# Optimization experiments

Hardware: AMD Instinct MI355X
Metric: run time of the kernel (lower is better)

Reference implementation:

```python
import jax, jax.numpy as jnp
import numpy as np

B, Nres, TOP_K, NUM_RBF = 2, 2048, 30, 16
MAX_REL = 32  # positional clip range -> 2*32+2 = 66 classes


def _gather_nodes(nodes, idx):
    # nodes: [B, N, ...], idx: [B, N, K] -> [B, N, K, ...]
    return jax.vmap(lambda n, i: n[i])(nodes, idx)


def _rbf(D):
    # D: [..., ] -> [..., NUM_RBF]; mu in [2, 22], sigma = 20/16
    mu = jnp.linspace(2.0, 22.0, NUM_RBF)
    sigma = (22.0 - 2.0) / NUM_RBF
    return jnp.exp(-(((D[..., None] - mu) / sigma) ** 2))


def setup_inputs() -> dict:
    key = jax.random.key(0)
    ks = jax.random.split(key, 4)
    X = jax.random.normal(ks[0], (B, Nres, 4, 3), dtype=jnp.float32) * 3.0
    mask = jnp.ones((B, Nres), dtype=jnp.float32)
    residue_idx = jnp.broadcast_to(jnp.arange(Nres, dtype=jnp.int32)[None], (B, Nres))
    chain_labels = jnp.zeros((B, Nres), dtype=jnp.int32)
    w_pos = jax.random.normal(ks[1], (66, 16), dtype=jnp.float32) * 0.05
    b_pos = jax.random.normal(ks[2], (16,), dtype=jnp.float32) * 0.05
    w_edge = jax.random.normal(ks[3], (416, 128), dtype=jnp.float32) * 0.05
    ln_gamma = jnp.ones((128,), dtype=jnp.float32)
    ln_beta = jnp.zeros((128,), dtype=jnp.float32)
    return dict(X=X, mask=mask, residue_idx=residue_idx, chain_labels=chain_labels,
                w_pos=w_pos, b_pos=b_pos, w_edge=w_edge, ln_gamma=ln_gamma, ln_beta=ln_beta)


def reference(X, mask, residue_idx, chain_labels, w_pos, b_pos, w_edge, ln_gamma, ln_beta):
    # virtual C-beta from N, C, Ca (atom order in X: N=0, C=1, Ca=2, O=3)
    b = X[:, :, 2, :] - X[:, :, 0, :]
    c = X[:, :, 1, :] - X[:, :, 2, :]
    a = jnp.cross(b, c)
    Cb = -0.58273431 * a + 0.56802827 * b - 0.54067466 * c + X[:, :, 2, :]
    N_, C, Ca, O = X[:, :, 0, :], X[:, :, 1, :], X[:, :, 2, :], X[:, :, 3, :]

    # masked kNN on C atoms (ProteinFeatures._dist)
    m2 = mask[:, None, :] * mask[:, :, None]                       # [B,N,N]
    dX = C[:, None, :, :] - C[:, :, None, :]
    D = m2 * jnp.sqrt(jnp.sum(dX ** 2, -1) + 1e-6)
    D_max = jnp.max(D, -1, keepdims=True)
    D_adj = D + (1.0 - m2) * D_max
    neg, E_idx = jax.lax.top_k(-D_adj, TOP_K)                      # smallest-k
    D_neighbors = -neg                                             # [B,N,K]

    # 25-channel RBF features; gather neighbor coords instead of NxN per pair
    atoms = jnp.stack([N_, Ca, Cb, C, O], 0)                       # [5,B,N,3]
    gathered = jax.vmap(lambda A: _gather_nodes(A, E_idx))(atoms)  # [5,B,N,K,3]
    # pair order follows torch source: NN,CaCa,CbCb,CN,CCa,CCb,NCa,NCb,CbCa,
    # NC,CaC,CbC,CaN,CbN,CaCb,OO,CO,OC,NO,ON,CbO,OCa,OCb,CaO  (0=N,1=Ca,2=Cb,3=C,4=O)
    pa = jnp.array([0, 1, 2, 3, 3, 3, 0, 0, 2, 0, 1, 2, 1, 2, 1, 4, 3, 4, 0, 4, 2, 4, 4, 1])
    pb = jnp.array([0, 1, 2, 0, 1, 2, 1, 2, 1, 3, 3, 3, 0, 0, 2, 4, 4, 3, 4, 0, 4, 1, 2, 4])
    A_sel = atoms[pa]                                              # [24,B,N,3]
    Bn_sel = gathered[pb]                                          # [24,B,N,K,3]
    Dp = jnp.sqrt(jnp.sum((A_sel[:, :, :, None, :] - Bn_sel) ** 2, -1) + 1e-6)
    RBF_all = jnp.concatenate([_rbf(D_neighbors)[None], _rbf(Dp)], 0)  # [25,B,N,K,16]
    RBF_all = jnp.moveaxis(RBF_all, 0, 3).reshape(B, Nres, TOP_K, 25 * NUM_RBF)

    # positional encodings over gathered offsets / chain match
    offset = residue_idx[:, :, None] - _gather_nodes(residue_idx, E_idx)   # [B,N,K]
    E_chains = (chain_labels[:, :, None] == _gather_nodes(chain_labels, E_idx)).astype(jnp.int32)
    d = jnp.clip(offset + MAX_REL, 0, 2 * MAX_REL) * E_chains + (1 - E_chains) * (2 * MAX_REL + 1)
    E_pos = w_pos[d] + b_pos                                       # one_hot @ W == gather

    # edge embedding + layernorm
    E = jnp.concatenate([E_pos, RBF_all], -1) @ w_edge             # [B,N,K,128]
    mu = E.mean(-1, keepdims=True)
    var = E.var(-1, keepdims=True)
    E = (E - mu) / jnp.sqrt(var + 1e-5) * ln_gamma + ln_beta
    return E, E_idx
```

## Files before the change

kernel.cpp:

```cpp
#include <hip/hip_runtime.h>
#include <hip/hip_bf16.h>
#include <stdint.h>

#define BB    2
#define NRES  2048
#define TOPK  30
#define NRBF  16
#define NFEAT 416
#define NCH   128
#define NS8   108
#define NKT   13
#define RPB   2

typedef __attribute__((ext_vector_type(4))) float f32x4;
typedef unsigned long long u64;

__constant__ int c_pa[24] = {0,1,2,3,3,3,0,0,2,0,1,2,1,2,1,4,3,4,0,4,2,4,4,1};
__constant__ int c_pb[24] = {0,1,2,0,1,2,1,2,1,3,3,3,0,0,2,4,4,3,4,0,4,1,2,4};

static __device__ __forceinline__ unsigned pack4_fp8(float f0, float f1, float f2, float f3) {
  unsigned r = 0;
  r = __builtin_amdgcn_cvt_pk_fp8_f32(f0, f1, r, false);
  r = __builtin_amdgcn_cvt_pk_fp8_f32(f2, f3, r, true);
  return r;
}
static __device__ __forceinline__ u64 umin64(u64 a, u64 b) { return a < b ? a : b; }
static __device__ __forceinline__ u64 umax64(u64 a, u64 b) { return a > b ? a : b; }

__global__ __launch_bounds__(256) void prep_kernel(const float* __restrict__ X,
                                                   const float* __restrict__ w_edge,
                                                   float* __restrict__ atoms,
                                                   float4* __restrict__ Cpk,
                                                   unsigned* __restrict__ wB8) {
  if (blockIdx.x < 16) {
    int id = blockIdx.x * 256 + threadIdx.x;
    const float* x = X + (size_t)id * 12;
    float nx = x[0], ny = x[1], nz = x[2];
    float cx = x[3], cy = x[4], cz = x[5];
    float ax = x[6], ay = x[7], az = x[8];
    float ox = x[9], oy = x[10], oz = x[11];
    float bx = ax - nx, by = ay - ny, bz = az - nz;
    float ccx = cx - ax, ccy = cy - ay, ccz = cz - az;
    float crx = by * ccz - bz * ccy;
    float cry = bz * ccx - bx * ccz;
    float crz = bx * ccy - by * ccx;
    float cbx = -0.58273431f * crx + 0.56802827f * bx - 0.54067466f * ccx + ax;
    float cby = -0.58273431f * cry + 0.56802827f * by - 0.54067466f * ccy + ay;
    float cbz = -0.58273431f * crz + 0.56802827f * bz - 0.54067466f * ccz + az;
    float* r = atoms + (size_t)id * 16;
    r[0] = nx;  r[1] = ny;  r[2] = nz;
    r[3] = ax;  r[4] = ay;  r[5] = az;
    r[6] = cbx; r[7] = cby; r[8] = cbz;
    r[9] = cx;  r[10] = cy; r[11] = cz;
    r[12] = ox; r[13] = oy; r[14] = oz;
    r[15] = 0.f;
    Cpk[id] = make_float4(cx, cy, cz, 0.f);
  } else {
    int id = (blockIdx.x - 16) * 256 + threadIdx.x;
    if (id >= NFEAT * NCH / 4) return;
    int bb   = id * 4;
    int j0   = bb & 7;
    int lane = (bb >> 3) & 63;
    int nt   = (bb >> 9) & 7;
    int kt   = bb >> 12;
    int col  = nt * 16 + (lane & 15);
    int kb   = kt * 32 + ((lane >> 4) << 3) + j0;
    wB8[id] = pack4_fp8(w_edge[(size_t)(kb + 0) * NCH + col],
                        w_edge[(size_t)(kb + 1) * NCH + col],
                        w_edge[(size_t)(kb + 2) * NCH + col],
                        w_edge[(size_t)(kb + 3) * NCH + col]);
  }
}

__global__ __launch_bounds__(256) void topk_kernel(const float4* __restrict__ Cpk,
                                                   int* __restrict__ eidx,
                                                   float* __restrict__ dn,
                                                   float* __restrict__ outI) {
  int tid = threadIdx.x;
  int lane = tid & 63;
  int bi = blockIdx.x * 4 + (tid >> 6);
  int b = bi >> 11;
  int i = bi & (NRES - 1);
  const float4* Cb = Cpk + (size_t)b * NRES;
  float4 ci = Cb[i];

  u64 key[4][8];
  u64 g1[4], g2[4];
#pragma unroll
  for (int g = 0; g < 4; ++g) {
    g1[g] = ~0ull; g2[g] = ~0ull;
#pragma unroll
    for (int s = 0; s < 8; ++s) {
      int j = lane + 64 * (g * 8 + s);
      float4 cj = Cb[j];
      float dx = cj.x - ci.x, dy = cj.y - ci.y, dz = cj.z - ci.z;
      float sm = __fadd_rn(__fadd_rn(__fadd_rn(__fmul_rn(dx, dx), __fmul_rn(dy, dy)),
                                     __fmul_rn(dz, dz)), 1e-6f);
      float d = sqrtf(sm);
      u64 kk = ((u64)__float_as_uint(d) << 32) | (unsigned)j;
      key[g][s] = kk;
      if (kk < g1[g]) { g2[g] = g1[g]; g1[g] = kk; }
      else if (kk < g2[g]) g2[g] = kk;
    }
  }

  for (int kk2 = 0; kk2 < TOPK / 2; ++kk2) {
    u64 x1 = umin64(g1[0], g1[1]);
    u64 x2 = umin64(umax64(g1[0], g1[1]), umin64(g2[0], g2[1]));
    u64 y1 = umin64(g1[2], g1[3]);
    u64 y2 = umin64(umax64(g1[2], g1[3]), umin64(g2[2], g2[3]));
    u64 m1 = umin64(x1, y1);
    u64 m2 = umin64(umax64(x1, y1), umin64(x2, y2));
#pragma unroll
    for (int off = 32; off; off >>= 1) {
      u64 o1 = __shfl_xor(m1, off, 64);
      u64 o2 = __shfl_xor(m2, off, 64);
      u64 n1 = umin64(m1, o1);
      u64 n2 = umin64(umax64(m1, o1), umin64(m2, o2));
      m1 = n1; m2 = n2;
    }
    if (lane == 0) {
      int i1 = (int)(unsigned)m1, i2 = (int)(unsigned)m2;
      size_t o = (size_t)bi * TOPK + 2 * kk2;
      eidx[o] = i1;           eidx[o + 1] = i2;
      dn[o]   = __uint_as_float((unsigned)(m1 >> 32));
      dn[o+1] = __uint_as_float((unsigned)(m2 >> 32));
      outI[o] = (float)i1;    outI[o + 1] = (float)i2;
    }
#pragma unroll
    for (int g = 0; g < 4; ++g) {
      bool hit = (g1[g] == m1) | (g1[g] == m2) | (g2[g] == m2);
      if (hit) {
        u64 n1 = ~0ull, n2 = ~0ull;
#pragma unroll
        for (int s = 0; s < 8; ++s) {
          u64 kv = key[g][s];
          if (kv == m1 || kv == m2) { kv = ~0ull; key[g][s] = kv; }
          if (kv < n1) { n2 = n1; n1 = kv; }
          else if (kv < n2) n2 = kv;
        }
        g1[g] = n1; g2[g] = n2;
      }
    }
  }
}

__global__ __launch_bounds__(256) void edge_mfma_kernel(
    const float* __restrict__ atoms, const int* __restrict__ eidx_g,
    const float* __restrict__ dn_g, const int* __restrict__ ridx,
    const int* __restrict__ chain, const float* __restrict__ w_pos,
    const float* __restrict__ b_pos, const unsigned* __restrict__ wB8,
    const float* __restrict__ gamma, const float* __restrict__ beta,
    float* __restrict__ outE) {
  __shared__ __align__(16) unsigned feat8[RPB * 32 * NS8];
  __shared__ float nat[RPB * TOPK][16];
  __shared__ float iat[RPB][16];
  __shared__ float dn_s[RPB * TOPK];
  __shared__ int   dsel[RPB * TOPK];
  __shared__ float2 lnp[RPB][32][4];

  int tid = threadIdx.x;
  int bi0 = blockIdx.x * RPB;
  int b = bi0 >> 11;
  int nq = tid >> 6, lane = tid & 63;
  int q = lane >> 4, ccol = lane & 15;

  if (tid < RPB * TOPK) {
    int gi = bi0 + tid / TOPK;
    int k = tid % TOPK;
    dn_s[tid] = dn_g[(size_t)gi * TOPK + k];
    int j = eidx_g[(size_t)gi * TOPK + k];
    int off = ridx[gi] - ridx[b * NRES + j];
    int ec = (chain[gi] == chain[b * NRES + j]) ? 1 : 0;
    int d = off + 32; d = d < 0 ? 0 : (d > 64 ? 64 : d);
    dsel[tid] = ec ? d : 65;
  }
  if (tid >= 64 && tid < 64 + RPB * 16) {
    int t = tid - 64;
    iat[t >> 4][t & 15] = atoms[((size_t)bi0 + (t >> 4)) * 16 + (t & 15)];
  }
  for (int idx = tid; idx < RPB * TOPK * 16; idx += 256) {
    int e = idx >> 4, f = idx & 15;
    int gi = bi0 + e / TOPK;
    nat[e][f] = atoms[((size_t)(b * NRES) + eidx_g[(size_t)gi * TOPK + (e % TOPK)]) * 16 + f];
  }
  for (int idx = tid; idx < RPB * 2 * NS8; idx += 256) {
    int r = idx / (2 * NS8), rem = idx % (2 * NS8);
    feat8[(r * 32 + 30) * NS8 + rem] = 0u;
  }
  __syncthreads();

  if (tid < RPB * TOPK * 4) {
    int e = tid >> 2, p = tid & 3;
    int f0 = p * 4, ds = dsel[e];
    int r = e / TOPK, k = e % TOPK;
    feat8[(r * 32 + k) * NS8 + p] = pack4_fp8(w_pos[ds * 16 + f0 + 0] + b_pos[f0 + 0],
                                              w_pos[ds * 16 + f0 + 1] + b_pos[f0 + 1],
                                              w_pos[ds * 16 + f0 + 2] + b_pos[f0 + 2],
                                              w_pos[ds * 16 + f0 + 3] + b_pos[f0 + 3]);
  }
  for (int idx = tid; idx < RPB * TOPK * 25; idx += 256) {
    int e = idx / 25, g = idx - e * 25;
    int r = e / TOPK, k = e - r * TOPK;
    float d;
    if (g == 0) {
      d = dn_s[e];
    } else {
      int qq = g - 1;
      const float* A  = &iat[r][c_pa[qq] * 3];
      const float* Bv = &nat[e][c_pb[qq] * 3];
      float dx = A[0] - Bv[0], dy = A[1] - Bv[1], dz = A[2] - Bv[2];
      d = sqrtf(dx * dx + dy * dy + dz * dz + 1e-6f);
    }
    float v[16];
#pragma unroll
    for (int j = 0; j < 16; ++j) {
      float mu = 2.0f + (float)j * (20.0f / 15.0f);
      float t = (d - mu) * 0.8f;
      v[j] = __expf(-t * t);
    }
    uint4 w4 = make_uint4(pack4_fp8(v[0], v[1], v[2], v[3]),
                          pack4_fp8(v[4], v[5], v[6], v[7]),
                          pack4_fp8(v[8], v[9], v[10], v[11]),
                          pack4_fp8(v[12], v[13], v[14], v[15]));
    *(uint4*)&feat8[(r * 32 + k) * NS8 + 4 + 4 * g] = w4;
  }
  __syncthreads();

  const unsigned* ar00 = &feat8[(0 * 32 + ccol) * NS8];
  const unsigned* ar01 = &feat8[(0 * 32 + 16 + ccol) * NS8];
  const unsigned* ar10 = &feat8[(1 * 32 + ccol) * NS8];
  const unsigned* ar11 = &feat8[(1 * 32 + 16 + ccol) * NS8];
  const u64* wBll = (const u64*)wB8;

  f32x4 a000 = {}, a001 = {}, a010 = {}, a011 = {};
  f32x4 a100 = {}, a101 = {}, a110 = {}, a111 = {};
#pragma unroll
  for (int kt = 0; kt < NKT; ++kt) {
    union { unsigned u[2]; long long l; } f00, f01, f10, f11;
    int ao = kt * 8 + q * 2;
    f00.u[0] = ar00[ao]; f00.u[1] = ar00[ao + 1];
    f01.u[0] = ar01[ao]; f01.u[1] = ar01[ao + 1];
    f10.u[0] = ar10[ao]; f10.u[1] = ar10[ao + 1];
    f11.u[0] = ar11[ao]; f11.u[1] = ar11[ao + 1];
    long long b0 = (long long)wBll[(size_t)(kt * 8 + nq * 2 + 0) * 64 + lane];
    long long b1 = (long long)wBll[(size_t)(kt * 8 + nq * 2 + 1) * 64 + lane];
    a000 = __builtin_amdgcn_mfma_f32_16x16x32_fp8_fp8(f00.l, b0, a000, 0, 0, 0);
    a001 = __builtin_amdgcn_mfma_f32_16x16x32_fp8_fp8(f00.l, b1, a001, 0, 0, 0);
    a010 = __builtin_amdgcn_mfma_f32_16x16x32_fp8_fp8(f01.l, b0, a010, 0, 0, 0);
    a011 = __builtin_amdgcn_mfma_f32_16x16x32_fp8_fp8(f01.l, b1, a011, 0, 0, 0);
    a100 = __builtin_amdgcn_mfma_f32_16x16x32_fp8_fp8(f10.l, b0, a100, 0, 0, 0);
    a101 = __builtin_amdgcn_mfma_f32_16x16x32_fp8_fp8(f10.l, b1, a101, 0, 0, 0);
    a110 = __builtin_amdgcn_mfma_f32_16x16x32_fp8_fp8(f11.l, b0, a110, 0, 0, 0);
    a111 = __builtin_amdgcn_mfma_f32_16x16x32_fp8_fp8(f11.l, b1, a111, 0, 0, 0);
  }

#pragma unroll
  for (int r = 0; r < RPB; ++r) {
#pragma unroll
    for (int mh = 0; mh < 2; ++mh) {
#pragma unroll
      for (int reg = 0; reg < 4; ++reg) {
        float v0, v1;
        if (r == 0) { v0 = mh ? a010[reg] : a000[reg]; v1 = mh ? a011[reg] : a001[reg]; }
        else        { v0 = mh ? a110[reg] : a100[reg]; v1 = mh ? a111[reg] : a101[reg]; }
        float s = v0 + v1, ss = v0 * v0 + v1 * v1;
        s  += __shfl_xor(s, 1, 64);  ss += __shfl_xor(ss, 1, 64);
        s  += __shfl_xor(s, 2, 64);  ss += __shfl_xor(ss, 2, 64);
        s  += __shfl_xor(s, 4, 64);  ss += __shfl_xor(ss, 4, 64);
        s  += __shfl_xor(s, 8, 64);  ss += __shfl_xor(ss, 8, 64);
        if (ccol == 0) lnp[r][(mh << 4) + q * 4 + reg][nq] = make_float2(s, ss);
      }
    }
  }
  __syncthreads();

  float g0 = gamma[(nq * 2 + 0) * 16 + ccol], be0 = beta[(nq * 2 + 0) * 16 + ccol];
  float g1 = gamma[(nq * 2 + 1) * 16 + ccol], be1 = beta[(nq * 2 + 1) * 16 + ccol];
#pragma unroll
  for (int r = 0; r < RPB; ++r) {
#pragma unroll
    for (int mh = 0; mh < 2; ++mh) {
#pragma unroll
      for (int reg = 0; reg < 4; ++reg) {
        int m = (mh << 4) + q * 4 + reg;
        if (m < TOPK) {
          float2 p0 = lnp[r][m][0], p1 = lnp[r][m][1], p2 = lnp[r][m][2], p3 = lnp[r][m][3];
          float s = (p0.x + p1.x) + (p2.x + p3.x);
          float ss = (p0.y + p1.y) + (p2.y + p3.y);
          float mu = s * (1.0f / 128.0f);
          float var = ss * (1.0f / 128.0f) - mu * mu;
          float rstd = rsqrtf(var + 1e-5f);
          float va, vb;
          if (r == 0) { va = mh ? a010[reg] : a000[reg]; vb = mh ? a011[reg] : a001[reg]; }
          else        { va = mh ? a110[reg] : a100[reg]; vb = mh ? a111[reg] : a101[reg]; }
          float* o = outE + ((size_t)(bi0 + r) * TOPK + m) * NCH + ccol;
          o[(nq * 2 + 0) * 16] = (va - mu) * rstd * g0 + be0;
          o[(nq * 2 + 1) * 16] = (vb - mu) * rstd * g1 + be1;
        }
      }
    }
  }
}

extern "C" void kernel_launch(void* const* d_in, const int* in_sizes, int n_in,
                              void* d_out, int out_size, void* d_ws, size_t ws_size,
                              hipStream_t stream) {
  const float* X      = (const float*)d_in[0];
  const int*   ridx   = (const int*)d_in[2];
  const int*   chain  = (const int*)d_in[3];
  const float* w_pos  = (const float*)d_in[4];
  const float* b_pos  = (const float*)d_in[5];
  const float* w_edge = (const float*)d_in[6];
  const float* gamma  = (const float*)d_in[7];
  const float* beta   = (const float*)d_in[8];

  float* outE = (float*)d_out;
  float* outI = outE + (size_t)BB * NRES * TOPK * NCH;

  char* p = (char*)d_ws;
  float* atoms = (float*)p;                 p += (size_t)BB * NRES * 16 * 4;
  int*   eidx  = (int*)p;                   p += (size_t)BB * NRES * TOPK * 4;
  float* dn    = (float*)p;                 p += (size_t)BB * NRES * TOPK * 4;
  unsigned* wB8 = (unsigned*)p;             p += (size_t)NCH * NFEAT;
  float4* Cpk  = (float4*)p;

  prep_kernel<<<16 + (NFEAT * NCH / 4 + 255) / 256, 256, 0, stream>>>(X, w_edge, atoms, Cpk, wB8);
  topk_kernel<<<BB * NRES / 4, 256, 0, stream>>>(Cpk, eidx, dn, outI);
  edge_mfma_kernel<<<BB * NRES / RPB, 256, 0, stream>>>(atoms, eidx, dn, ridx, chain,
                                                        w_pos, b_pos, wB8, gamma, beta, outE);
}
```

Baseline: 93.81 us.

## Process two query rows per wave in top-k and switch to single-min extraction

Each wavefront in the top-k kernel now handles two query residues, sharing the neighbor coordinate loads, and interleaves their two independent shuffle-reduction chains. Selection goes from extracting two minima per round with a top-2 merge to extracting one minimum per round over 30 rounds, which makes each round simpler. The intent is better instruction-level parallelism and fewer loads per query. The cost is double the key register footprint, raised occupancy pressure (a launch_bounds min-blocks hint of 2 is added), twice as many reduction rounds, and half as many blocks.

```diff
diff --git a/kernel.cpp b/kernel.cpp
--- a/kernel.cpp
+++ b/kernel.cpp
@@ -24,8 +24,6 @@
   r = __builtin_amdgcn_cvt_pk_fp8_f32(f2, f3, r, true);
   return r;
 }
-static __device__ __forceinline__ u64 umin64(u64 a, u64 b) { return a < b ? a : b; }
-static __device__ __forceinline__ u64 umax64(u64 a, u64 b) { return a > b ? a : b; }
 
 __global__ __launch_bounds__(256) void prep_kernel(const float* __restrict__ X,
                                                    const float* __restrict__ w_edge,
@@ -72,74 +70,84 @@
   }
 }
 
-__global__ __launch_bounds__(256) void topk_kernel(const float4* __restrict__ Cpk,
-                                                   int* __restrict__ eidx,
-                                                   float* __restrict__ dn,
-                                                   float* __restrict__ outI) {
+__global__ __launch_bounds__(256, 2) void topk_kernel(const float4* __restrict__ Cpk,
+                                                      int* __restrict__ eidx,
+                                                      float* __restrict__ dn,
+                                                      float* __restrict__ outI) {
   int tid = threadIdx.x;
   int lane = tid & 63;
-  int bi = blockIdx.x * 4 + (tid >> 6);
-  int b = bi >> 11;
-  int i = bi & (NRES - 1);
+  int biA = blockIdx.x * 8 + (tid >> 6) * 2;
+  int biB = biA + 1;
+  int b = biA >> 11;
   const float4* Cb = Cpk + (size_t)b * NRES;
-  float4 ci = Cb[i];
-
-  u64 key[4][8];
-  u64 g1[4], g2[4];
+  float4 ciA = Cb[biA & (NRES - 1)];
+  float4 ciB = Cb[biB & (NRES - 1)];
+
+  u64 keyA[4][8], keyB[4][8];
+  u64 subA[4], subB[4];
 #pragma unroll
   for (int g = 0; g < 4; ++g) {
-    g1[g] = ~0ull; g2[g] = ~0ull;
+    subA[g] = ~0ull; subB[g] = ~0ull;
 #pragma unroll
     for (int s = 0; s < 8; ++s) {
       int j = lane + 64 * (g * 8 + s);
       float4 cj = Cb[j];
-      float dx = cj.x - ci.x, dy = cj.y - ci.y, dz = cj.z - ci.z;
-      float sm = __fadd_rn(__fadd_rn(__fadd_rn(__fmul_rn(dx, dx), __fmul_rn(dy, dy)),
-                                     __fmul_rn(dz, dz)), 1e-6f);
-      float d = sqrtf(sm);
-      u64 kk = ((u64)__float_as_uint(d) << 32) | (unsigned)j;
-      key[g][s] = kk;
-      if (kk < g1[g]) { g2[g] = g1[g]; g1[g] = kk; }
-      else if (kk < g2[g]) g2[g] = kk;
-    }
-  }
-
-  for (int kk2 = 0; kk2 < TOPK / 2; ++kk2) {
-    u64 x1 = umin64(g1[0], g1[1]);
-    u64 x2 = umin64(umax64(g1[0], g1[1]), umin64(g2[0], g2[1]));
-    u64 y1 = umin64(g1[2], g1[3]);
-    u64 y2 = umin64(umax64(g1[2], g1[3]), umin64(g2[2], g2[3]));
-    u64 m1 = umin64(x1, y1);
-    u64 m2 = umin64(umax64(x1, y1), umin64(x2, y2));
+      float dxA = cj.x - ciA.x, dyA = cj.y - ciA.y, dzA = cj.z - ciA.z;
+      float dxB = cj.x - ciB.x, dyB = cj.y - ciB.y, dzB = cj.z - ciB.z;
+      float smA = __fadd_rn(__fadd_rn(__fadd_rn(__fmul_rn(dxA, dxA), __fmul_rn(dyA, dyA)),
+                                      __fmul_rn(dzA, dzA)), 1e-6f);
+      float smB = __fadd_rn(__fadd_rn(__fadd_rn(__fmul_rn(dxB, dxB), __fmul_rn(dyB, dyB)),
+                                      __fmul_rn(dzB, dzB)), 1e-6f);
+      float dA = sqrtf(smA), dB = sqrtf(smB);
+      u64 kA = ((u64)__float_as_uint(dA) << 32) | (unsigned)j;
+      u64 kB = ((u64)__float_as_uint(dB) << 32) | (unsigned)j;
+      keyA[g][s] = kA; keyB[g][s] = kB;
+      if (kA < subA[g]) subA[g] = kA;
+      if (kB < subB[g]) subB[g] = kB;
+    }
+  }
+
+  for (int k = 0; k < TOPK; ++k) {
+    u64 a01 = subA[0] < subA[1] ? subA[0] : subA[1];
+    u64 a23 = subA[2] < subA[3] ? subA[2] : subA[3];
+    u64 gmA = a01 < a23 ? a01 : a23;
+    u64 b01 = subB[0] < subB[1] ? subB[0] : subB[1];
+    u64 b23 = subB[2] < subB[3] ? subB[2] : subB[3];
+    u64 gmB = b01 < b23 ? b01 : b23;
 #pragma unroll
     for (int off = 32; off; off >>= 1) {
-      u64 o1 = __shfl_xor(m1, off, 64);
-      u64 o2 = __shfl_xor(m2, off, 64);
-      u64 n1 = umin64(m1, o1);
-      u64 n2 = umin64(umax64(m1, o1), umin64(m2, o2));
-      m1 = n1; m2 = n2;
+      u64 oA = __shfl_xor(gmA, off, 64);
+      u64 oB = __shfl_xor(gmB, off, 64);
+      if (oA < gmA) gmA = oA;
+      if (oB < gmB) gmB = oB;
     }
     if (lane == 0) {
-      int i1 = (int)(unsigned)m1, i2 = (int)(unsigned)m2;
-      size_t o = (size_t)bi * TOPK + 2 * kk2;
-      eidx[o] = i1;           eidx[o + 1] = i2;
-      dn[o]   = __uint_as_float((unsigned)(m1 >> 32));
-      dn[o+1] = __uint_as_float((unsigned)(m2 >> 32));
-      outI[o] = (float)i1;    outI[o + 1] = (float)i2;
+      int iA = (int)(unsigned)(gmA & 0xffffffffu);
+      int iB = (int)(unsigned)(gmB & 0xffffffffu);
+      eidx[(size_t)biA * TOPK + k] = iA;
+      eidx[(size_t)biB * TOPK + k] = iB;
+      dn[(size_t)biA * TOPK + k] = __uint_as_float((unsigned)(gmA >> 32));
+      dn[(size_t)biB * TOPK + k] = __uint_as_float((unsigned)(gmB >> 32));
+      outI[(size_t)biA * TOPK + k] = (float)iA;
+      outI[(size_t)biB * TOPK + k] = (float)iB;
     }
 #pragma unroll
     for (int g = 0; g < 4; ++g) {
-      bool hit = (g1[g] == m1) | (g1[g] == m2) | (g2[g] == m2);
-      if (hit) {
-        u64 n1 = ~0ull, n2 = ~0ull;
+      if (subA[g] == gmA) {
+        subA[g] = ~0ull;
 #pragma unroll
         for (int s = 0; s < 8; ++s) {
-          u64 kv = key[g][s];
-          if (kv == m1 || kv == m2) { kv = ~0ull; key[g][s] = kv; }
-          if (kv < n1) { n2 = n1; n1 = kv; }
-          else if (kv < n2) n2 = kv;
+          if (keyA[g][s] == gmA) keyA[g][s] = ~0ull;
+          if (keyA[g][s] < subA[g]) subA[g] = keyA[g][s];
         }
-        g1[g] = n1; g2[g] = n2;
+      }
+      if (subB[g] == gmB) {
+        subB[g] = ~0ull;
+#pragma unroll
+        for (int s = 0; s < 8; ++s) {
+          if (keyB[g][s] == gmB) keyB[g][s] = ~0ull;
+          if (keyB[g][s] < subB[g]) subB[g] = keyB[g][s];
+        }
       }
     }
   }
@@ -326,7 +334,7 @@
   float4* Cpk  = (float4*)p;
 
   prep_kernel<<<16 + (NFEAT * NCH / 4 + 255) / 256, 256, 0, stream>>>(X, w_edge, atoms, Cpk, wB8);
-  topk_kernel<<<BB * NRES / 4, 256, 0, stream>>>(Cpk, eidx, dn, outI);
+  topk_kernel<<<BB * NRES / 8, 256, 0, stream>>>(Cpk, eidx, dn, outI);
   edge_mfma_kernel<<<BB * NRES / RPB, 256, 0, stream>>>(atoms, eidx, dn, ridx, chain,
                                                         w_pos, b_pos, wB8, gamma, beta, outE);
 }
```

New measurement: 87.44 us. 1.07x faster.

## Fuse top-k neighbor search into edge MFMA kernel with four residues per block

Applied to the files above, without the earlier changes.

Merges the separate top-k kernel into the edge-embedding kernel. Each of the four waves in a block now computes the 30 nearest neighbors of one residue and writes indices and distances straight to shared memory, which removes the global eidx/dn round trip and one kernel launch. Residues per block rise from 2 to 4 so the four waves match four residues, and the MFMA loop is generalised over RPB with more accumulators. The top-k selection is also simplified from extracting two minima per reduction round to one, which doubles the number of cross-lane shuffle reductions. The larger accumulator set and LDS footprint may reduce occupancy.

```diff
diff --git a/kernel.cpp b/kernel.cpp
--- a/kernel.cpp
+++ b/kernel.cpp
@@ -10,7 +10,7 @@
 #define NCH   128
 #define NS8   108
 #define NKT   13
-#define RPB   2
+#define RPB   4
 
 typedef __attribute__((ext_vector_type(4))) float f32x4;
 typedef unsigned long long u64;
@@ -24,8 +24,6 @@
   r = __builtin_amdgcn_cvt_pk_fp8_f32(f2, f3, r, true);
   return r;
 }
-static __device__ __forceinline__ u64 umin64(u64 a, u64 b) { return a < b ? a : b; }
-static __device__ __forceinline__ u64 umax64(u64 a, u64 b) { return a > b ? a : b; }
 
 __global__ __launch_bounds__(256) void prep_kernel(const float* __restrict__ X,
                                                    const float* __restrict__ w_edge,
@@ -72,126 +70,104 @@
   }
 }
 
-__global__ __launch_bounds__(256) void topk_kernel(const float4* __restrict__ Cpk,
-                                                   int* __restrict__ eidx,
-                                                   float* __restrict__ dn,
-                                                   float* __restrict__ outI) {
-  int tid = threadIdx.x;
-  int lane = tid & 63;
-  int bi = blockIdx.x * 4 + (tid >> 6);
-  int b = bi >> 11;
-  int i = bi & (NRES - 1);
-  const float4* Cb = Cpk + (size_t)b * NRES;
-  float4 ci = Cb[i];
-
-  u64 key[4][8];
-  u64 g1[4], g2[4];
-#pragma unroll
-  for (int g = 0; g < 4; ++g) {
-    g1[g] = ~0ull; g2[g] = ~0ull;
-#pragma unroll
-    for (int s = 0; s < 8; ++s) {
-      int j = lane + 64 * (g * 8 + s);
-      float4 cj = Cb[j];
-      float dx = cj.x - ci.x, dy = cj.y - ci.y, dz = cj.z - ci.z;
-      float sm = __fadd_rn(__fadd_rn(__fadd_rn(__fmul_rn(dx, dx), __fmul_rn(dy, dy)),
-                                     __fmul_rn(dz, dz)), 1e-6f);
-      float d = sqrtf(sm);
-      u64 kk = ((u64)__float_as_uint(d) << 32) | (unsigned)j;
-      key[g][s] = kk;
-      if (kk < g1[g]) { g2[g] = g1[g]; g1[g] = kk; }
-      else if (kk < g2[g]) g2[g] = kk;
-    }
-  }
-
-  for (int kk2 = 0; kk2 < TOPK / 2; ++kk2) {
-    u64 x1 = umin64(g1[0], g1[1]);
-    u64 x2 = umin64(umax64(g1[0], g1[1]), umin64(g2[0], g2[1]));
-    u64 y1 = umin64(g1[2], g1[3]);
-    u64 y2 = umin64(umax64(g1[2], g1[3]), umin64(g2[2], g2[3]));
-    u64 m1 = umin64(x1, y1);
-    u64 m2 = umin64(umax64(x1, y1), umin64(x2, y2));
-#pragma unroll
-    for (int off = 32; off; off >>= 1) {
-      u64 o1 = __shfl_xor(m1, off, 64);
-      u64 o2 = __shfl_xor(m2, off, 64);
-      u64 n1 = umin64(m1, o1);
-      u64 n2 = umin64(umax64(m1, o1), umin64(m2, o2));
-      m1 = n1; m2 = n2;
-    }
-    if (lane == 0) {
-      int i1 = (int)(unsigned)m1, i2 = (int)(unsigned)m2;
-      size_t o = (size_t)bi * TOPK + 2 * kk2;
-      eidx[o] = i1;           eidx[o + 1] = i2;
-      dn[o]   = __uint_as_float((unsigned)(m1 >> 32));
-      dn[o+1] = __uint_as_float((unsigned)(m2 >> 32));
-      outI[o] = (float)i1;    outI[o + 1] = (float)i2;
-    }
-#pragma unroll
-    for (int g = 0; g < 4; ++g) {
-      bool hit = (g1[g] == m1) | (g1[g] == m2) | (g2[g] == m2);
-      if (hit) {
-        u64 n1 = ~0ull, n2 = ~0ull;
-#pragma unroll
-        for (int s = 0; s < 8; ++s) {
-          u64 kv = key[g][s];
-          if (kv == m1 || kv == m2) { kv = ~0ull; key[g][s] = kv; }
-          if (kv < n1) { n2 = n1; n1 = kv; }
-          else if (kv < n2) n2 = kv;
-        }
-        g1[g] = n1; g2[g] = n2;
-      }
-    }
-  }
-}
-
-__global__ __launch_bounds__(256) void edge_mfma_kernel(
-    const float* __restrict__ atoms, const int* __restrict__ eidx_g,
-    const float* __restrict__ dn_g, const int* __restrict__ ridx,
-    const int* __restrict__ chain, const float* __restrict__ w_pos,
-    const float* __restrict__ b_pos, const unsigned* __restrict__ wB8,
+__global__ __launch_bounds__(256) void fused_kernel(
+    const float* __restrict__ atoms, const float4* __restrict__ Cpk,
+    const int* __restrict__ ridx, const int* __restrict__ chain,
+    const float* __restrict__ w_pos, const float* __restrict__ b_pos,
+    const unsigned* __restrict__ wB8,
     const float* __restrict__ gamma, const float* __restrict__ beta,
-    float* __restrict__ outE) {
+    float* __restrict__ outE, float* __restrict__ outI) {
   __shared__ __align__(16) unsigned feat8[RPB * 32 * NS8];
   __shared__ float nat[RPB * TOPK][16];
   __shared__ float iat[RPB][16];
   __shared__ float dn_s[RPB * TOPK];
+  __shared__ int   eidx_s[RPB * TOPK];
   __shared__ int   dsel[RPB * TOPK];
   __shared__ float2 lnp[RPB][32][4];
 
   int tid = threadIdx.x;
+  int w = tid >> 6, lane = tid & 63;
   int bi0 = blockIdx.x * RPB;
   int b = bi0 >> 11;
-  int nq = tid >> 6, lane = tid & 63;
   int q = lane >> 4, ccol = lane & 15;
 
+  for (int idx = tid; idx < RPB * 2 * NS8; idx += 256) {
+    int r = idx / (2 * NS8), rem = idx % (2 * NS8);
+    feat8[(r * 32 + 30) * NS8 + rem] = 0u;
+  }
+
+  {
+    int bi = bi0 + w;
+    const float4* Cb = Cpk + (size_t)b * NRES;
+    float4 ci = Cb[bi & (NRES - 1)];
+    u64 key[4][8];
+    u64 sub[4];
+#pragma unroll
+    for (int g = 0; g < 4; ++g) {
+      sub[g] = ~0ull;
+#pragma unroll
+      for (int s = 0; s < 8; ++s) {
+        int j = lane + 64 * (g * 8 + s);
+        float4 cj = Cb[j];
+        float dx = cj.x - ci.x, dy = cj.y - ci.y, dz = cj.z - ci.z;
+        float sm = __fadd_rn(__fadd_rn(__fadd_rn(__fmul_rn(dx, dx), __fmul_rn(dy, dy)),
+                                       __fmul_rn(dz, dz)), 1e-6f);
+        float d = sqrtf(sm);
+        key[g][s] = ((u64)__float_as_uint(d) << 32) | (unsigned)j;
+        if (key[g][s] < sub[g]) sub[g] = key[g][s];
+      }
+    }
+    for (int k = 0; k < TOPK; ++k) {
+      u64 m01 = sub[0] < sub[1] ? sub[0] : sub[1];
+      u64 m23 = sub[2] < sub[3] ? sub[2] : sub[3];
+      u64 gm = m01 < m23 ? m01 : m23;
+#pragma unroll
+      for (int off = 32; off; off >>= 1) {
+        u64 o = __shfl_xor(gm, off, 64);
+        if (o < gm) gm = o;
+      }
+      if (lane == 0) {
+        int idx = (int)(unsigned)(gm & 0xffffffffu);
+        eidx_s[w * TOPK + k] = idx;
+        dn_s[w * TOPK + k] = __uint_as_float((unsigned)(gm >> 32));
+        outI[(size_t)bi * TOPK + k] = (float)idx;
+      }
+#pragma unroll
+      for (int g = 0; g < 4; ++g) {
+        if (sub[g] == gm) {
+          sub[g] = ~0ull;
+#pragma unroll
+          for (int s = 0; s < 8; ++s) {
+            if (key[g][s] == gm) key[g][s] = ~0ull;
+            if (key[g][s] < sub[g]) sub[g] = key[g][s];
+          }
+        }
+      }
+    }
+  }
+  __syncthreads();
+
   if (tid < RPB * TOPK) {
-    int gi = bi0 + tid / TOPK;
-    int k = tid % TOPK;
-    dn_s[tid] = dn_g[(size_t)gi * TOPK + k];
-    int j = eidx_g[(size_t)gi * TOPK + k];
+    int e = tid;
+    int gi = bi0 + e / TOPK;
+    int j = eidx_s[e];
     int off = ridx[gi] - ridx[b * NRES + j];
     int ec = (chain[gi] == chain[b * NRES + j]) ? 1 : 0;
     int d = off + 32; d = d < 0 ? 0 : (d > 64 ? 64 : d);
-    dsel[tid] = ec ? d : 65;
-  }
-  if (tid >= 64 && tid < 64 + RPB * 16) {
-    int t = tid - 64;
+    dsel[e] = ec ? d : 65;
+  }
+  if (tid >= 128 && tid < 128 + RPB * 16) {
+    int t = tid - 128;
     iat[t >> 4][t & 15] = atoms[((size_t)bi0 + (t >> 4)) * 16 + (t & 15)];
   }
   for (int idx = tid; idx < RPB * TOPK * 16; idx += 256) {
     int e = idx >> 4, f = idx & 15;
-    int gi = bi0 + e / TOPK;
-    nat[e][f] = atoms[((size_t)(b * NRES) + eidx_g[(size_t)gi * TOPK + (e % TOPK)]) * 16 + f];
-  }
-  for (int idx = tid; idx < RPB * 2 * NS8; idx += 256) {
-    int r = idx / (2 * NS8), rem = idx % (2 * NS8);
-    feat8[(r * 32 + 30) * NS8 + rem] = 0u;
-  }
-  __syncthreads();
-
-  if (tid < RPB * TOPK * 4) {
-    int e = tid >> 2, p = tid & 3;
+    nat[e][f] = atoms[((size_t)(b * NRES) + eidx_s[e]) * 16 + f];
+  }
+  __syncthreads();
+
+  for (int idx = tid; idx < RPB * TOPK * 4; idx += 256) {
+    int e = idx >> 2, p = idx & 3;
     int f0 = p * 4, ds = dsel[e];
     int r = e / TOPK, k = e % TOPK;
     feat8[(r * 32 + k) * NS8 + p] = pack4_fp8(w_pos[ds * 16 + f0 + 0] + b_pos[f0 + 0],
@@ -227,32 +203,26 @@
   }
   __syncthreads();
 
-  const unsigned* ar00 = &feat8[(0 * 32 + ccol) * NS8];
-  const unsigned* ar01 = &feat8[(0 * 32 + 16 + ccol) * NS8];
-  const unsigned* ar10 = &feat8[(1 * 32 + ccol) * NS8];
-  const unsigned* ar11 = &feat8[(1 * 32 + 16 + ccol) * NS8];
   const u64* wBll = (const u64*)wB8;
-
-  f32x4 a000 = {}, a001 = {}, a010 = {}, a011 = {};
-  f32x4 a100 = {}, a101 = {}, a110 = {}, a111 = {};
+  f32x4 acc[RPB][2][2] = {};
+  int nq = w;
 #pragma unroll
   for (int kt = 0; kt < NKT; ++kt) {
-    union { unsigned u[2]; long long l; } f00, f01, f10, f11;
-    int ao = kt * 8 + q * 2;
-    f00.u[0] = ar00[ao]; f00.u[1] = ar00[ao + 1];
-    f01.u[0] = ar01[ao]; f01.u[1] = ar01[ao + 1];
-    f10.u[0] = ar10[ao]; f10.u[1] = ar10[ao + 1];
-    f11.u[0] = ar11[ao]; f11.u[1] = ar11[ao + 1];
     long long b0 = (long long)wBll[(size_t)(kt * 8 + nq * 2 + 0) * 64 + lane];
     long long b1 = (long long)wBll[(size_t)(kt * 8 + nq * 2 + 1) * 64 + lane];
-    a000 = __builtin_amdgcn_mfma_f32_16x16x32_fp8_fp8(f00.l, b0, a000, 0, 0, 0);
-    a001 = __builtin_amdgcn_mfma_f32_16x16x32_fp8_fp8(f00.l, b1, a001, 0, 0, 0);
-    a010 = __builtin_amdgcn_mfma_f32_16x16x32_fp8_fp8(f01.l, b0, a010, 0, 0, 0);
-    a011 = __builtin_amdgcn_mfma_f32_16x16x32_fp8_fp8(f01.l, b1, a011, 0, 0, 0);
-    a100 = __builtin_amdgcn_mfma_f32_16x16x32_fp8_fp8(f10.l, b0, a100, 0, 0, 0);
-    a101 = __builtin_amdgcn_mfma_f32_16x16x32_fp8_fp8(f10.l, b1, a101, 0, 0, 0);
-    a110 = __builtin_amdgcn_mfma_f32_16x16x32_fp8_fp8(f11.l, b0, a110, 0, 0, 0);
-    a111 = __builtin_amdgcn_mfma_f32_16x16x32_fp8_fp8(f11.l, b1, a111, 0, 0, 0);
+    int ao = kt * 8 + q * 2;
+#pragma unroll
+    for (int r = 0; r < RPB; ++r) {
+      union { unsigned u[2]; long long l; } f0, f1;
+      const unsigned* a0 = &feat8[(r * 32 + ccol) * NS8];
+      const unsigned* a1 = &feat8[(r * 32 + 16 + ccol) * NS8];
+      f0.u[0] = a0[ao]; f0.u[1] = a0[ao + 1];
+      f1.u[0] = a1[ao]; f1.u[1] = a1[ao + 1];
+      acc[r][0][0] = __builtin_amdgcn_mfma_f32_16x16x32_fp8_fp8(f0.l, b0, acc[r][0][0], 0, 0, 0);
+      acc[r][0][1] = __builtin_amdgcn_mfma_f32_16x16x32_fp8_fp8(f0.l, b1, acc[r][0][1], 0, 0, 0);
+      acc[r][1][0] = __builtin_amdgcn_mfma_f32_16x16x32_fp8_fp8(f1.l, b0, acc[r][1][0], 0, 0, 0);
+      acc[r][1][1] = __builtin_amdgcn_mfma_f32_16x16x32_fp8_fp8(f1.l, b1, acc[r][1][1], 0, 0, 0);
+    }
   }
 
 #pragma unroll
@@ -261,9 +231,8 @@
     for (int mh = 0; mh < 2; ++mh) {
 #pragma unroll
       for (int reg = 0; reg < 4; ++reg) {
-        float v0, v1;
-        if (r == 0) { v0 = mh ? a010[reg] : a000[reg]; v1 = mh ? a011[reg] : a001[reg]; }
-        else        { v0 = mh ? a110[reg] : a100[reg]; v1 = mh ? a111[reg] : a101[reg]; }
+        float v0 = acc[r][mh][0][reg];
+        float v1 = acc[r][mh][1][reg];
         float s = v0 + v1, ss = v0 * v0 + v1 * v1;
         s  += __shfl_xor(s, 1, 64);  ss += __shfl_xor(ss, 1, 64);
         s  += __shfl_xor(s, 2, 64);  ss += __shfl_xor(ss, 2, 64);
@@ -291,9 +260,8 @@
           float mu = s * (1.0f / 128.0f);
           float var = ss * (1.0f / 128.0f) - mu * mu;
           float rstd = rsqrtf(var + 1e-5f);
-          float va, vb;
-          if (r == 0) { va = mh ? a010[reg] : a000[reg]; vb = mh ? a011[reg] : a001[reg]; }
-          else        { va = mh ? a110[reg] : a100[reg]; vb = mh ? a111[reg] : a101[reg]; }
+          float va = acc[r][mh][0][reg];
+          float vb = acc[r][mh][1][reg];
           float* o = outE + ((size_t)(bi0 + r) * TOPK + m) * NCH + ccol;
           o[(nq * 2 + 0) * 16] = (va - mu) * rstd * g0 + be0;
           o[(nq * 2 + 1) * 16] = (vb - mu) * rstd * g1 + be1;
@@ -320,13 +288,11 @@
 
   char* p = (char*)d_ws;
   float* atoms = (float*)p;                 p += (size_t)BB * NRES * 16 * 4;
-  int*   eidx  = (int*)p;                   p += (size_t)BB * NRES * TOPK * 4;
-  float* dn    = (float*)p;                 p += (size_t)BB * NRES * TOPK * 4;
   unsigned* wB8 = (unsigned*)p;             p += (size_t)NCH * NFEAT;
   float4* Cpk  = (float4*)p;
 
   prep_kernel<<<16 + (NFEAT * NCH / 4 + 255) / 256, 256, 0, stream>>>(X, w_edge, atoms, Cpk, wB8);
-  topk_kernel<<<BB * NRES / 4, 256, 0, stream>>>(Cpk, eidx, dn, outI);
-  edge_mfma_kernel<<<BB * NRES / RPB, 256, 0, stream>>>(atoms, eidx, dn, ridx, chain,
-                                                        w_pos, b_pos, wB8, gamma, beta, outE);
-}
+  fused_kernel<<<BB * NRES / RPB, 256, 0, stream>>>(atoms, Cpk, ridx, chain,
+                                                    w_pos, b_pos, wB8, gamma, beta,
+                                                    outE, outI);
+}
```

Result: slower. 99.14 us (+5.7%).
